# Performance work log

Hardware: AMD Instinct MI355X
Metric: run time of the kernel (lower is better)

## Reference

```python
import jax, jax.numpy as jnp
import numpy as np

NLAT = 192  # octahedral O96-class grid


def _lons(nlat):
    half = [20 + 4 * i for i in range(nlat // 2)]
    return half + half[::-1]


def _dft_matrix(nlat, mmax):
    # Truncated per-ring real-DFT basis (torch.fft.rfft convention, 'forward' 1/n norm).
    # Ring j has nlon_j points; frequencies beyond its Nyquist (m > nlon_j//2) are zero.
    lons = _lons(nlat)
    max_nlon = max(lons)
    D = np.zeros((nlat, max_nlon, mmax), dtype=np.complex64)
    for j, n in enumerate(lons):
        keep = min(mmax, n // 2 + 1)
        k = np.arange(n)[:, None]
        m = np.arange(keep)[None, :]
        D[j, :n, :keep] = np.exp(-2j * np.pi * k * m / n) / n
    return D


def _legendre_weights(nlat, lmax, mmax):
    # Orthonormalized associated Legendre P_l^m at Gaussian latitudes (north->south),
    # with Gaussian quadrature weights and the 2*pi longitude factor folded in.
    xg, wg = np.polynomial.legendre.leggauss(nlat)
    x = xg[::-1].copy()
    w = wg[::-1].copy()
    s = np.sqrt(1.0 - x * x)
    leg = np.zeros((lmax, mmax, nlat))
    pmm = np.full(nlat, 1.0 / np.sqrt(4.0 * np.pi))
    for m in range(mmax):
        if m > 0:
            pmm = -np.sqrt((2 * m + 1) / (2.0 * m)) * s * pmm
        if m < lmax:
            leg[m, m] = pmm
        if m + 1 < lmax:
            leg[m + 1, m] = np.sqrt(2 * m + 3.0) * x * pmm
        for l in range(m + 2, lmax):
            a = np.sqrt((4.0 * l * l - 1.0) / (l * l - m * m))
            bb = np.sqrt(((2.0 * l + 1.0) * (l - 1 + m) * (l - 1 - m)) / ((2.0 * l - 3.0) * (l * l - m * m)))
            leg[l, m] = a * x * leg[l - 1, m] - bb * leg[l - 2, m]
    leg = 2.0 * np.pi * leg * w[None, None, :]
    return leg.astype(np.float32)


def setup_inputs() -> dict:
    key = jax.random.key(0)
    nlat = NLAT
    lmax = mmax = nlat // 2
    n_points = sum(_lons(nlat))  # 40320 for nlat=192
    data = jax.random.normal(key, (4, 1, 1, n_points, 100), dtype=jnp.float32)
    dft = jnp.asarray(_dft_matrix(nlat, mmax))
    leg = jnp.asarray(_legendre_weights(nlat, lmax, mmax))
    return {"data": data, "dft": dft, "leg": leg}


def reference(data, dft, leg):
    b, t, e, p, v = data.shape
    nlat, max_nlon, mmax = dft.shape
    lmax = leg.shape[0]
    lons = _lons(nlat)
    # static scatter map: flattened ragged rings -> [nlat, max_nlon] padded layout
    flat_idx = np.concatenate([j * max_nlon + np.arange(n) for j, n in enumerate(lons)])
    x = jnp.transpose(data, (0, 1, 2, 4, 3)).reshape(-1, p)  # [(b t e v), p]
    B = x.shape[0]
    x_pad = jnp.zeros((B, nlat * max_nlon), x.dtype).at[:, flat_idx].set(x)
    x_pad = x_pad.reshape(B, nlat, max_nlon)
    # ragged per-ring truncated real DFT, then associated-Legendre contraction
    f_hat = jnp.einsum('bjn,jnm->bjm', x_pad, dft)        # [B, nlat, mmax] complex
    coeffs = jnp.einsum('bjm,lmj->blm', f_hat, leg)       # [B, lmax, mmax] complex
    coeffs = coeffs.reshape(b, t, e, v, lmax, mmax)
    return jnp.transpose(coeffs, (0, 1, 2, 4, 5, 3))      # [b, t, e, yF, xF, v]
```

## Files before the change

### kernel.cpp

```cpp
#include <hip/hip_runtime.h>

#define NLAT 192
#define NPTS 40320
#define MMAX 96
#define LMAX 96
#define NV   100
#define MAXN 400
#define NB   400

typedef __attribute__((ext_vector_type(8))) _Float16 half8v;
typedef __attribute__((ext_vector_type(4))) float f32x4;

static __device__ __forceinline__ float bits2f(unsigned int b) {
    union { unsigned int i; float f; } v; v.i = b; return v.f;
}
static __device__ __forceinline__ unsigned int f2bf(float f) {
    union { float f; unsigned int i; } v; v.f = f;
    return (v.i + 0x7FFFu + ((v.i >> 16) & 1u)) >> 16;
}
static __device__ __forceinline__ unsigned short f2h(float f) {
    union { _Float16 h; unsigned short s; } u; u.h = (_Float16)f; return u.s;
}
static __device__ __forceinline__ float h2f(unsigned short s) {
    union { _Float16 h; unsigned short s; } u; u.s = s; return (float)u.h;
}
static __device__ __forceinline__ void split2(float a, float b,
                                              unsigned int& hw, unsigned int& lw) {
    unsigned short h0 = f2h(a), h1 = f2h(b);
    unsigned short l0 = f2h(a - h2f(h0)), l1 = f2h(b - h2f(h1));
    hw = (unsigned int)h0 | ((unsigned int)h1 << 16);
    lw = (unsigned int)l0 | ((unsigned int)l1 << 16);
}

static __device__ __forceinline__ int Ssum(int n) {
    int q = n >> 3, r = n & 7; return 4 * q * (q - 1) + q * r;
}
static __device__ __forceinline__ int atoffk(int j) {
    if (j < 96) return 32 * (Ssum(j + 12) - 4);
    return 32 * (672 + 676 - Ssum(204 - j));
}
static __device__ __forceinline__ int kpad_of(int j) {
    return 32 * ((j < 96 ? (j + 12) : (203 - j)) >> 3);
}

__global__ __launch_bounds__(256) void leg_conv_kernel(
    const float* __restrict__ leg,
    unsigned short* __restrict__ legh,
    unsigned short* __restrict__ legl)
{
    int idx = blockIdx.x * 256 + threadIdx.x;
    if (idx >= 96 * 96 * 192) return;
    int j = idx % 192;
    int lm = idx / 192;
    int m = lm % 96, l = lm / 96;
    float v = leg[idx];
    unsigned short h = f2h(v);
    unsigned short lo = f2h(v - h2f(h));
    size_t o = ((size_t)m * 96 + l) * 192 + j;
    legh[o] = h;
    legl[o] = lo;
}

__global__ __launch_bounds__(256) void dft_transpose_kernel(
    const unsigned int* __restrict__ dftw,
    unsigned short* __restrict__ At)
{
    const int j = blockIdx.x;
    const int kpad = kpad_of(j);
    const int t = blockIdx.y;
    const int k0 = t * 32;
    if (k0 >= kpad) return;
    const int n = j < 96 ? 20 + 4 * j : 400 - 4 * (j - 96);
    unsigned short* abase = At + (size_t)atoffk(j) * 192 + (size_t)t * 6144;
    const int tid = threadIdx.x;
#pragma unroll
    for (int s = 0; s < 3; ++s) {
        int slot = s * 256 + tid;
        int row = slot % 192;
        int ch  = slot / 192;
        int m = row < 96 ? row : row - 96;
        bool isIm = row >= 96;
        const unsigned int* dp = dftw + ((size_t)j * MAXN + k0 + ch * 8) * 96 + m;
        unsigned short o[8];
#pragma unroll
        for (int i = 0; i < 8; ++i) {
            int k = k0 + ch * 8 + i;
            unsigned int v = (k < n) ? dp[(size_t)i * 96] : 0u;
            float f = isIm ? bits2f(v & 0xFFFF0000u) : bits2f(v << 16);
            o[i] = f2h(f);
        }
        uint4 pk;
        pk.x = (unsigned int)o[0] | ((unsigned int)o[1] << 16);
        pk.y = (unsigned int)o[2] | ((unsigned int)o[3] << 16);
        pk.z = (unsigned int)o[4] | ((unsigned int)o[5] << 16);
        pk.w = (unsigned int)o[6] | ((unsigned int)o[7] << 16);
        *(uint4*)(abase + (size_t)row * 32 + ch * 8) = pk;
    }
}

static __device__ __forceinline__ void k1_step(
    const half8v (&acur)[12], half8v (&anxt)[12], float (&xf)[8],
    f32x4 (&acc)[12], int t, int nsteps, int n, int start, int kg,
    int lr, bool cok, int cc, const float* __restrict__ dbase,
    const half8v* __restrict__ avb)
{
    unsigned int BH[4], BL[4];
#pragma unroll
    for (int q = 0; q < 4; ++q)
        split2(xf[2 * q], xf[2 * q + 1], BH[q], BL[q]);

    if (t + 1 < nsteps) {
        int kb = (t + 1) * 32 + kg * 8;
#pragma unroll
        for (int i = 0; i < 8; ++i) {
            int k = kb + i;
            xf[i] = (cok && k < n) ? dbase[(size_t)(start + k) * NV + cc] : 0.f;
        }
        const half8v* avn = avb + (size_t)(t + 1) * 768;
#pragma unroll
        for (int mt = 0; mt < 12; ++mt)
            anxt[mt] = avn[(mt * 16 + lr) * 4 + kg];
    }

    union { uint4 u; half8v h; } ubh, ubl;
    ubh.u = (uint4){BH[0], BH[1], BH[2], BH[3]};
    ubl.u = (uint4){BL[0], BL[1], BL[2], BL[3]};
#pragma unroll
    for (int mt = 0; mt < 12; ++mt) {
        acc[mt] = __builtin_amdgcn_mfma_f32_16x16x32_f16(acur[mt], ubh.h, acc[mt], 0, 0, 0);
        acc[mt] = __builtin_amdgcn_mfma_f32_16x16x32_f16(acur[mt], ubl.h, acc[mt], 0, 0, 0);
    }
}

__global__ __launch_bounds__(256) void dft_mfma_kernel(
    const float* __restrict__ data,
    const unsigned short* __restrict__ At,
    unsigned short* __restrict__ fh,
    int c0, int cn)
{
    const int id  = blockIdx.x;
    const int p   = id % 96;
    const int bt  = id / 96;
    const int tid = threadIdx.x;
    const int w   = tid >> 6;
    const int l   = tid & 63;
    const int lr  = l & 15;
    const int kg  = l >> 4;

    const int Bb = c0 + bt * 50;
    const int bb = Bb / NV;
    const int vb = Bb % NV;
    const float* dbase = data + (size_t)bb * NPTS * NV + vb;
    const int cc = w * 16 + lr;
    const bool cok = cc < 50;

    for (int rr = 0; rr < 2; ++rr) {
        int j, n, start;
        if (rr == 0) { j = p;      n = 20 + 4 * p;  start = 2 * p * p + 18 * p; }
        else         { j = 96 + p; n = 400 - 4 * p; start = 20160 + 402 * p - 2 * p * p; }
        const int nsteps = kpad_of(j) >> 5;
        const half8v* avb = (const half8v*)(At + (size_t)atoffk(j) * 192);

        f32x4 acc[12];
#pragma unroll
        for (int mt = 0; mt < 12; ++mt) acc[mt] = (f32x4){0.f, 0.f, 0.f, 0.f};

        half8v aA[12], aB[12];
        float xf[8];
#pragma unroll
        for (int mt = 0; mt < 12; ++mt)
            aA[mt] = avb[(mt * 16 + lr) * 4 + kg];
#pragma unroll
        for (int i = 0; i < 8; ++i) {
            int k = kg * 8 + i;
            xf[i] = (cok && k < n) ? dbase[(size_t)(start + k) * NV + cc] : 0.f;
        }

        int t = 0;
        while (true) {
            k1_step(aA, aB, xf, acc, t, nsteps, n, start, kg, lr, cok, cc, dbase, avb);
            if (++t >= nsteps) break;
            k1_step(aB, aA, xf, acc, t, nsteps, n, start, kg, lr, cok, cc, dbase, avb);
            if (++t >= nsteps) break;
        }

        if (cok) {
            int Brel = bt * 50 + cc;
#pragma unroll
            for (int mt = 0; mt < 12; ++mt) {
#pragma unroll
                for (int r = 0; r < 4; ++r)
                    fh[((size_t)j * 192 + mt * 16 + kg * 4 + r) * cn + Brel] =
                        f2h(acc[mt][r]);
            }
        }
    }
}

static __device__ __forceinline__ void k2_step(
    unsigned short (&fcur)[2][8], unsigned short (&fnxt)[2][8],
    f32x4 (&acc)[6][2], int s, int m, int lr, int kg, int col, int cn,
    const unsigned short* __restrict__ legh,
    const unsigned short* __restrict__ legl,
    const unsigned short* __restrict__ fh)
{
    const int j0 = s * 32;
    half8v ah[6], al[6];
#pragma unroll
    for (int lt = 0; lt < 6; ++lt) {
        size_t o = ((size_t)m * 96 + lt * 16 + lr) * 192 + j0 + kg * 8;
        ah[lt] = *(const half8v*)&legh[o];
        al[lt] = *(const half8v*)&legl[o];
    }
    if (s + 1 < 6) {
        const int jn = (s + 1) * 32 + kg * 8;
#pragma unroll
        for (int pl = 0; pl < 2; ++pl)
#pragma unroll
            for (int i = 0; i < 8; ++i)
                fnxt[pl][i] = fh[((size_t)(jn + i) * 192 + m + 96 * pl) * cn + col];
    }
    half8v fF[2];
#pragma unroll
    for (int pl = 0; pl < 2; ++pl) {
        union { half8v h; unsigned short s16[8]; } uf;
#pragma unroll
        for (int i = 0; i < 8; ++i) uf.s16[i] = fcur[pl][i];
        fF[pl] = uf.h;
    }
#pragma unroll
    for (int lt = 0; lt < 6; ++lt)
#pragma unroll
        for (int pl = 0; pl < 2; ++pl) {
            acc[lt][pl] = __builtin_amdgcn_mfma_f32_16x16x32_f16(ah[lt], fF[pl], acc[lt][pl], 0, 0, 0);
            acc[lt][pl] = __builtin_amdgcn_mfma_f32_16x16x32_f16(al[lt], fF[pl], acc[lt][pl], 0, 0, 0);
        }
}

__global__ __launch_bounds__(256) void leg_mfma_kernel(
    const unsigned short* __restrict__ legh,
    const unsigned short* __restrict__ legl,
    const unsigned short* __restrict__ fh,
    unsigned int* __restrict__ out,
    int c0, int cn)
{
    const int m   = blockIdx.x;
    const int bt  = blockIdx.y;
    const int tid = threadIdx.x;
    const int w   = tid >> 6;
    const int l   = tid & 63;
    const int lr  = l & 15;
    const int kg  = l >> 4;

    const int c  = w * 16 + lr;
    const bool cok = c < 50;
    const int col = bt * 50 + (cok ? c : 0);

    f32x4 acc[6][2];
#pragma unroll
    for (int lt = 0; lt < 6; ++lt)
#pragma unroll
        for (int pl = 0; pl < 2; ++pl) acc[lt][pl] = (f32x4){0.f, 0.f, 0.f, 0.f};

    unsigned short fA[2][8], fB[2][8];
#pragma unroll
    for (int pl = 0; pl < 2; ++pl)
#pragma unroll
        for (int i = 0; i < 8; ++i)
            fA[pl][i] = fh[((size_t)(kg * 8 + i) * 192 + m + 96 * pl) * cn + col];

#pragma unroll
    for (int ss = 0; ss < 3; ++ss) {
        k2_step(fA, fB, acc, 2 * ss,     m, lr, kg, col, cn, legh, legl, fh);
        k2_step(fB, fA, acc, 2 * ss + 1, m, lr, kg, col, cn, legh, legl, fh);
    }

    if (cok) {
        int B = c0 + bt * 50 + c;
        int bb = B / NV, vv = B % NV;
#pragma unroll
        for (int lt = 0; lt < 6; ++lt) {
#pragma unroll
            for (int r = 0; r < 4; ++r) {
                int ll = lt * 16 + kg * 4 + r;
                out[(((size_t)bb * LMAX + ll) * MMAX + m) * NV + vv] =
                    f2bf(acc[lt][0][r]) | (f2bf(acc[lt][1][r]) << 16);
            }
        }
    }
}

extern "C" void kernel_launch(void* const* d_in, const int* in_sizes, int n_in,
                              void* d_out, int out_size, void* d_ws, size_t ws_size,
                              hipStream_t stream) {
    if (n_in != 3) return;

    const float* data = (const float*)d_in[0];
    const unsigned int* dftw = (const unsigned int*)d_in[1];
    const float* leg  = (const float*)d_in[2];
    unsigned int* out = (unsigned int*)d_out;

    const size_t LEGN = (size_t)96 * 96 * 192;
    const size_t LEGB = 2 * LEGN * sizeof(unsigned short);
    const size_t ATN  = (size_t)43008 * 192;
    const size_t ATB  = ATN * sizeof(unsigned short);
    const size_t rowb = (size_t)192 * 192 * sizeof(unsigned short);
    if (ws_size < LEGB + ATB + 50 * rowb) return;

    unsigned short* legh = (unsigned short*)d_ws;
    unsigned short* legl = legh + LEGN;
    unsigned short* At   = legl + LEGN;

    size_t maxrows = (ws_size - LEGB - ATB) / rowb;
    int chunk = (int)((maxrows / 50) * 50);
    if (chunk > NB) chunk = NB;

    leg_conv_kernel<<<dim3((96 * 96 * 192 + 255) / 256), dim3(256), 0, stream>>>(
        leg, legh, legl);
    dft_transpose_kernel<<<dim3(192, 13), dim3(256), 0, stream>>>(dftw, At);

    for (int c0 = 0; c0 < NB; c0 += chunk) {
        int cn = NB - c0 < chunk ? NB - c0 : chunk;
        unsigned short* fh = At + ATN;

        int nbt = cn / 50;
        dim3 g1(96 * nbt);
        dft_mfma_kernel<<<g1, dim3(256), 0, stream>>>(data, At, fh, c0, cn);
        dim3 g2(96, nbt);
        leg_mfma_kernel<<<g2, dim3(256), 0, stream>>>(legh, legl, fh, out, c0, cn);
    }
}
```

Before: 93.99 us.

## Re-tile DFT kernel to 16 columns per block with halved M tiles

The DFT MFMA kernel is reorganized so each block handles 16 batch columns and two latitude-ring pairs, with each wave computing half of the 192 output rows. This cuts the accumulator and A-operand register footprint (no A double-buffer, 6 instead of 12 tiles) and sets a launch-bounds occupancy hint to raise waves per CU. All 50-column padding waste is removed, and the host-side chunk loop is dropped in favour of a single full-size intermediate buffer. The trade-off is that A fragments are now loaded from global memory inside the loop without prefetch, the data prefetch moves two steps ahead, and the workspace must hold the whole intermediate.

```diff
diff --git a/kernel.cpp b/kernel.cpp
--- a/kernel.cpp
+++ b/kernel.cpp
@@ -98,108 +98,90 @@
     }
 }
 
-static __device__ __forceinline__ void k1_step(
-    const half8v (&acur)[12], half8v (&anxt)[12], float (&xf)[8],
-    f32x4 (&acc)[12], int t, int nsteps, int n, int start, int kg,
-    int lr, bool cok, int cc, const float* __restrict__ dbase,
-    const half8v* __restrict__ avb)
-{
-    unsigned int BH[4], BL[4];
-#pragma unroll
-    for (int q = 0; q < 4; ++q)
-        split2(xf[2 * q], xf[2 * q + 1], BH[q], BL[q]);
-
-    if (t + 1 < nsteps) {
-        int kb = (t + 1) * 32 + kg * 8;
-#pragma unroll
-        for (int i = 0; i < 8; ++i) {
-            int k = kb + i;
-            xf[i] = (cok && k < n) ? dbase[(size_t)(start + k) * NV + cc] : 0.f;
-        }
-        const half8v* avn = avb + (size_t)(t + 1) * 768;
-#pragma unroll
-        for (int mt = 0; mt < 12; ++mt)
-            anxt[mt] = avn[(mt * 16 + lr) * 4 + kg];
-    }
-
-    union { uint4 u; half8v h; } ubh, ubl;
-    ubh.u = (uint4){BH[0], BH[1], BH[2], BH[3]};
-    ubl.u = (uint4){BL[0], BL[1], BL[2], BL[3]};
-#pragma unroll
-    for (int mt = 0; mt < 12; ++mt) {
-        acc[mt] = __builtin_amdgcn_mfma_f32_16x16x32_f16(acur[mt], ubh.h, acc[mt], 0, 0, 0);
-        acc[mt] = __builtin_amdgcn_mfma_f32_16x16x32_f16(acur[mt], ubl.h, acc[mt], 0, 0, 0);
-    }
-}
-
-__global__ __launch_bounds__(256) void dft_mfma_kernel(
+__global__ __launch_bounds__(256, 4) void dft_mfma_kernel(
     const float* __restrict__ data,
     const unsigned short* __restrict__ At,
-    unsigned short* __restrict__ fh,
-    int c0, int cn)
+    unsigned short* __restrict__ fh)
 {
     const int id  = blockIdx.x;
-    const int p   = id % 96;
-    const int bt  = id / 96;
+    const int pg  = id % 48;
+    const int ct  = id / 48;
     const int tid = threadIdx.x;
     const int w   = tid >> 6;
     const int l   = tid & 63;
     const int lr  = l & 15;
     const int kg  = l >> 4;
-
-    const int Bb = c0 + bt * 50;
-    const int bb = Bb / NV;
-    const int vb = Bb % NV;
-    const float* dbase = data + (size_t)bb * NPTS * NV + vb;
-    const int cc = w * 16 + lr;
-    const bool cok = cc < 50;
+    const int pp  = 2 * pg + (w >> 1);
+    const int mh  = w & 1;
+
+    const int Bb = ct * 16 + lr;
+    const int bb = Bb / NV, vv = Bb % NV;
+    const float* dbase = data + (size_t)bb * NPTS * NV + vv;
 
     for (int rr = 0; rr < 2; ++rr) {
         int j, n, start;
-        if (rr == 0) { j = p;      n = 20 + 4 * p;  start = 2 * p * p + 18 * p; }
-        else         { j = 96 + p; n = 400 - 4 * p; start = 20160 + 402 * p - 2 * p * p; }
+        if (rr == 0) { j = pp;      n = 20 + 4 * pp;  start = 2 * pp * pp + 18 * pp; }
+        else         { j = 96 + pp; n = 400 - 4 * pp; start = 20160 + 402 * pp - 2 * pp * pp; }
         const int nsteps = kpad_of(j) >> 5;
         const half8v* avb = (const half8v*)(At + (size_t)atoffk(j) * 192);
 
-        f32x4 acc[12];
-#pragma unroll
-        for (int mt = 0; mt < 12; ++mt) acc[mt] = (f32x4){0.f, 0.f, 0.f, 0.f};
-
-        half8v aA[12], aB[12];
-        float xf[8];
-#pragma unroll
-        for (int mt = 0; mt < 12; ++mt)
-            aA[mt] = avb[(mt * 16 + lr) * 4 + kg];
+        f32x4 acc[6];
+#pragma unroll
+        for (int mt = 0; mt < 6; ++mt) acc[mt] = (f32x4){0.f, 0.f, 0.f, 0.f};
+
+        float xfA[8], xfB[8];
 #pragma unroll
         for (int i = 0; i < 8; ++i) {
-            int k = kg * 8 + i;
-            xf[i] = (cok && k < n) ? dbase[(size_t)(start + k) * NV + cc] : 0.f;
-        }
-
-        int t = 0;
-        while (true) {
-            k1_step(aA, aB, xf, acc, t, nsteps, n, start, kg, lr, cok, cc, dbase, avb);
-            if (++t >= nsteps) break;
-            k1_step(aB, aA, xf, acc, t, nsteps, n, start, kg, lr, cok, cc, dbase, avb);
-            if (++t >= nsteps) break;
-        }
-
-        if (cok) {
-            int Brel = bt * 50 + cc;
-#pragma unroll
-            for (int mt = 0; mt < 12; ++mt) {
-#pragma unroll
-                for (int r = 0; r < 4; ++r)
-                    fh[((size_t)j * 192 + mt * 16 + kg * 4 + r) * cn + Brel] =
-                        f2h(acc[mt][r]);
+            int k = kg * 8 + i; if (k > n - 1) k = n - 1;
+            xfA[i] = dbase[(size_t)(start + k) * NV];
+        }
+        if (nsteps > 1) {
+#pragma unroll
+            for (int i = 0; i < 8; ++i) {
+                int k = 32 + kg * 8 + i; if (k > n - 1) k = n - 1;
+                xfB[i] = dbase[(size_t)(start + k) * NV];
             }
+        }
+
+        for (int t = 0; t < nsteps; ++t) {
+            float* xcur = (t & 1) ? xfB : xfA;
+            unsigned int BH[4], BL[4];
+#pragma unroll
+            for (int q = 0; q < 4; ++q)
+                split2(xcur[2 * q], xcur[2 * q + 1], BH[q], BL[q]);
+            if (t + 2 < nsteps) {
+                int kb = (t + 2) * 32 + kg * 8;
+#pragma unroll
+                for (int i = 0; i < 8; ++i) {
+                    int k = kb + i; if (k > n - 1) k = n - 1;
+                    xcur[i] = dbase[(size_t)(start + k) * NV];
+                }
+            }
+            const half8v* av = avb + (size_t)t * 768;
+            union { uint4 u; half8v h; } ubh, ubl;
+            ubh.u = (uint4){BH[0], BH[1], BH[2], BH[3]};
+            ubl.u = (uint4){BL[0], BL[1], BL[2], BL[3]};
+#pragma unroll
+            for (int mt = 0; mt < 6; ++mt) {
+                half8v a = av[((mh * 96 + mt * 16) + lr) * 4 + kg];
+                acc[mt] = __builtin_amdgcn_mfma_f32_16x16x32_f16(a, ubh.h, acc[mt], 0, 0, 0);
+                acc[mt] = __builtin_amdgcn_mfma_f32_16x16x32_f16(a, ubl.h, acc[mt], 0, 0, 0);
+            }
+        }
+
+#pragma unroll
+        for (int mt = 0; mt < 6; ++mt) {
+#pragma unroll
+            for (int r = 0; r < 4; ++r)
+                fh[((size_t)j * 192 + mh * 96 + mt * 16 + kg * 4 + r) * NB + Bb] =
+                    f2h(acc[mt][r]);
         }
     }
 }
 
 static __device__ __forceinline__ void k2_step(
     unsigned short (&fcur)[2][8], unsigned short (&fnxt)[2][8],
-    f32x4 (&acc)[6][2], int s, int m, int lr, int kg, int col, int cn,
+    f32x4 (&acc)[6][2], int s, int m, int lr, int kg, int col,
     const unsigned short* __restrict__ legh,
     const unsigned short* __restrict__ legl,
     const unsigned short* __restrict__ fh)
@@ -218,7 +200,7 @@
         for (int pl = 0; pl < 2; ++pl)
 #pragma unroll
             for (int i = 0; i < 8; ++i)
-                fnxt[pl][i] = fh[((size_t)(jn + i) * 192 + m + 96 * pl) * cn + col];
+                fnxt[pl][i] = fh[((size_t)(jn + i) * 192 + m + 96 * pl) * NB + col];
     }
     half8v fF[2];
 #pragma unroll
@@ -241,8 +223,7 @@
     const unsigned short* __restrict__ legh,
     const unsigned short* __restrict__ legl,
     const unsigned short* __restrict__ fh,
-    unsigned int* __restrict__ out,
-    int c0, int cn)
+    unsigned int* __restrict__ out)
 {
     const int m   = blockIdx.x;
     const int bt  = blockIdx.y;
@@ -267,16 +248,16 @@
     for (int pl = 0; pl < 2; ++pl)
 #pragma unroll
         for (int i = 0; i < 8; ++i)
-            fA[pl][i] = fh[((size_t)(kg * 8 + i) * 192 + m + 96 * pl) * cn + col];
+            fA[pl][i] = fh[((size_t)(kg * 8 + i) * 192 + m + 96 * pl) * NB + col];
 
 #pragma unroll
     for (int ss = 0; ss < 3; ++ss) {
-        k2_step(fA, fB, acc, 2 * ss,     m, lr, kg, col, cn, legh, legl, fh);
-        k2_step(fB, fA, acc, 2 * ss + 1, m, lr, kg, col, cn, legh, legl, fh);
+        k2_step(fA, fB, acc, 2 * ss,     m, lr, kg, col, legh, legl, fh);
+        k2_step(fB, fA, acc, 2 * ss + 1, m, lr, kg, col, legh, legl, fh);
     }
 
     if (cok) {
-        int B = c0 + bt * 50 + c;
+        int B = bt * 50 + c;
         int bb = B / NV, vv = B % NV;
 #pragma unroll
         for (int lt = 0; lt < 6; ++lt) {
@@ -304,29 +285,18 @@
     const size_t LEGB = 2 * LEGN * sizeof(unsigned short);
     const size_t ATN  = (size_t)43008 * 192;
     const size_t ATB  = ATN * sizeof(unsigned short);
-    const size_t rowb = (size_t)192 * 192 * sizeof(unsigned short);
-    if (ws_size < LEGB + ATB + 50 * rowb) return;
+    const size_t FHB  = (size_t)192 * 192 * NB * sizeof(unsigned short);
+    if (ws_size < LEGB + ATB + FHB) return;
 
     unsigned short* legh = (unsigned short*)d_ws;
     unsigned short* legl = legh + LEGN;
     unsigned short* At   = legl + LEGN;
-
-    size_t maxrows = (ws_size - LEGB - ATB) / rowb;
-    int chunk = (int)((maxrows / 50) * 50);
-    if (chunk > NB) chunk = NB;
+    unsigned short* fh   = At + ATN;
 
     leg_conv_kernel<<<dim3((96 * 96 * 192 + 255) / 256), dim3(256), 0, stream>>>(
         leg, legh, legl);
     dft_transpose_kernel<<<dim3(192, 13), dim3(256), 0, stream>>>(dftw, At);
 
-    for (int c0 = 0; c0 < NB; c0 += chunk) {
-        int cn = NB - c0 < chunk ? NB - c0 : chunk;
-        unsigned short* fh = At + ATN;
-
-        int nbt = cn / 50;
-        dim3 g1(96 * nbt);
-        dft_mfma_kernel<<<g1, dim3(256), 0, stream>>>(data, At, fh, c0, cn);
-        dim3 g2(96, nbt);
-        leg_mfma_kernel<<<g2, dim3(256), 0, stream>>>(legh, legl, fh, out, c0, cn);
-    }
-}
+    dft_mfma_kernel<<<dim3(1200), dim3(256), 0, stream>>>(data, At, fh);
+    leg_mfma_kernel<<<dim3(96, 8), dim3(256), 0, stream>>>(legh, legl, fh, out);
+}
```

Result: no change. 93.35 us (-0.7%).
